# Kernel optimization log

Measured on AMD Instinct MI355X. Metric: run time of the kernel, lower is better.

Reference implementation:

```python
import jax, jax.numpy as jnp
import numpy as np

B = 64        # num_groups
G = 32        # group_size
D = 2000      # output dim (counts per bin/gene)
M = 16        # m_samples
E = 16        # noise_dim
DIN = 256
LAM = 1.0
TRUST = 0.25
SMOOTH = 1e-8
IPF_ITERS = 60
EPS = 1e-12


def _arch(x, noise, W, b):
    # simple linear architecture: concat(x, noise) @ W + b
    return jnp.concatenate([x, noise], axis=-1) @ W + b


def _loss(x, target, W, b, noise_loss):
    # replicate each row m times (unsqueeze(1).expand(...).reshape == repeat)
    x_rep = jnp.repeat(x, M, axis=0)                      # [n*M, DIN]
    pred = _arch(x_rep, noise_loss, W, b)                 # [n*M, D] (no act_fn in loss path)
    pred = pred.reshape(B, G, M, D).sum(axis=1)           # [B, M, D]
    term_conf = jnp.linalg.norm(pred - target[:, None, :], axis=2).mean(axis=1)  # [B]
    sq = jnp.sum(pred * pred, axis=2)                     # [B, M]
    inn = jnp.einsum('bmd,bnd->bmn', pred, pred)          # [B, M, M]
    sqd = jnp.clip(sq[:, :, None] + sq[:, None, :] - 2.0 * inn, 1e-6)
    d = jnp.sqrt(sqd)
    mask = 1.0 - jnp.eye(M, dtype=d.dtype)
    mean_pd = jnp.sum(d * mask, axis=(1, 2)) / (M * (M - 1))
    return jnp.mean(term_conf - (LAM / 2.0) * mean_pd)


def _ipf(x_pred, C):
    # KL/I-projection with row anchoring (keep_rows=True, trust_clip=0.25)
    y = jnp.clip(x_pred, 0.0)
    C = jnp.clip(C.astype(y.dtype), 0.0)
    R = y.sum(axis=2)                                     # [B, G] anchor row totals
    col_zero = (y.sum(axis=1) <= 0) & (C > 0)
    y = y + SMOOTH * col_zero[:, None, :].astype(y.dtype)
    row_zero = (y.sum(axis=2) <= 0) & (R > 0)
    y = y + SMOOTH * row_zero[:, :, None].astype(y.dtype)

    def body(_, y):
        col = jnp.clip(y.sum(axis=1), EPS)
        y = y * jnp.clip(C / col, 1.0 - TRUST, 1.0 + TRUST)[:, None, :]
        row = jnp.clip(y.sum(axis=2), EPS)
        y = y * jnp.clip(R / row, 1.0 - TRUST, 1.0 + TRUST)[:, :, None]
        return y

    y = jax.lax.fori_loop(0, IPF_ITERS, body, y)
    col = jnp.clip(y.sum(axis=1), EPS)
    return y * (C / col)[:, None, :]


def _rank(v, descending):
    # rank along last axis via double argsort (0 = first picked)
    order = jnp.argsort(-v if descending else v, axis=-1)
    return jnp.argsort(order, axis=-1)


def _round_to_targets(x, target_bd):
    # exact integerization across G per (B, D); jit-safe full-G rank replaces dynamic-k topk+scatter
    x = jnp.clip(x, 0.0)
    xf = jnp.floor(x)
    y = xf.astype(jnp.int32)                              # [B, G, D]
    frac = x - xf
    need = target_bd - y.sum(axis=1)                      # [B, D]
    pos = jnp.clip(need, 0)
    q = pos // G
    y = y + q[:, None, :]
    r = pos - q * G
    rank = _rank(jnp.transpose(frac, (0, 2, 1)), descending=True)   # [B, D, G]
    add = (rank < r[:, :, None]).astype(jnp.int32)
    y = y + jnp.transpose(add, (0, 2, 1))
    # negative residuals: remove from smallest frac among y > 0
    need = target_bd - y.sum(axis=1)
    neg = jnp.clip(-need, 0)
    neg = jnp.minimum(neg, y.sum(axis=1))
    q = neg // G
    y_before = y
    y = jnp.clip(y - q[:, None, :], 0)
    removed = (y_before - y).sum(axis=1)
    r = neg - removed
    frac_m = jnp.where(y > 0, frac, jnp.inf)
    rank = _rank(jnp.transpose(frac_m, (0, 2, 1)), descending=False)
    rem = (rank < r[:, :, None]).astype(jnp.int32)
    y = jnp.clip(y - jnp.transpose(rem, (0, 2, 1)), 0)
    return y


def setup_inputs() -> dict:
    key = jax.random.key(0)
    ks = jax.random.split(key, 6)
    x = jax.random.normal(ks[0], (B * G, DIN), dtype=jnp.float32)
    target = jax.random.uniform(ks[1], (B, D), dtype=jnp.float32) * 100.0
    target_sum = jax.random.randint(ks[2], (B, D), 0, 200, dtype=jnp.int32)
    W = jax.random.normal(ks[3], (DIN + E, D), dtype=jnp.float32) * 0.02
    b = jnp.zeros((D,), dtype=jnp.float32)
    noise_loss = jax.random.normal(ks[4], (B * G * M, E), dtype=jnp.float32)
    noise_sample = jax.random.normal(ks[5], (B * G, E), dtype=jnp.float32)
    return {"x": x, "target": target, "target_sum": target_sum, "W": W, "b": b,
            "noise_loss": noise_loss, "noise_sample": noise_sample}


def reference(x, target, target_sum, W, b, noise_loss, noise_sample):
    loss = _loss(x, target, W, b, noise_loss)
    # conditional_sample pipeline (no-grad in original): softplus act (min_value==0)
    x_pred = jax.nn.softplus(_arch(x, noise_sample, W, b)).reshape(B, G, D)
    y_float = _ipf(x_pred, target_sum.astype(jnp.float32))
    y_int = _round_to_targets(y_float, target_sum.astype(jnp.int32))
    return loss, y_int.reshape(B * G, D)
```

## Files before the change

### kernel.cpp

```cpp
#include <hip/hip_runtime.h>
#include <math.h>

#define NB   64
#define NG   32
#define ND   2000
#define NM   16
#define NE   16
#define NDIN 256
#define NK   272

__device__ __forceinline__ float clampf(float v, float lo, float hi) {
    return fminf(fmaxf(v, lo), hi);
}

__device__ __forceinline__ float softplusf(float v) {
    return (v > 20.f) ? v : log1pf(expf(v));
}

__device__ __forceinline__ float readlane_f(float v, int lane) {
    return __int_as_float(__builtin_amdgcn_readlane(__float_as_int(v), lane));
}

__device__ __forceinline__ float wave_sum32(float v[NG], int lane) {
    {   const bool hi = (lane & 32) != 0;
        #pragma unroll
        for (int k = 0; k < 16; ++k) {
            float s = hi ? v[k] : v[k + 16];
            float r = __shfl_xor(s, 32);
            v[k] = (hi ? v[k + 16] : v[k]) + r;
        }
    }
    {   const bool hi = (lane & 16) != 0;
        #pragma unroll
        for (int k = 0; k < 8; ++k) {
            float s = hi ? v[k] : v[k + 8];
            float r = __shfl_xor(s, 16);
            v[k] = (hi ? v[k + 8] : v[k]) + r;
        }
    }
    {   const bool hi = (lane & 8) != 0;
        #pragma unroll
        for (int k = 0; k < 4; ++k) {
            float s = hi ? v[k] : v[k + 4];
            float r = __shfl_xor(s, 8);
            v[k] = (hi ? v[k + 4] : v[k]) + r;
        }
    }
    {   const bool hi = (lane & 4) != 0;
        #pragma unroll
        for (int k = 0; k < 2; ++k) {
            float s = hi ? v[k] : v[k + 2];
            float r = __shfl_xor(s, 4);
            v[k] = (hi ? v[k + 2] : v[k]) + r;
        }
    }
    {   const bool hi = (lane & 2) != 0;
        float s = hi ? v[0] : v[1];
        float r = __shfl_xor(s, 2);
        v[0] = (hi ? v[1] : v[0]) + r;
    }
    v[0] += __shfl_xor(v[0], 1);
    return v[0];
}


__device__ __forceinline__ void ipf_path(
        const float* __restrict__ xp, const int* __restrict__ tsum,
        float* __restrict__ out, float* smem, int b, int t) {
    const int lane = t & 63, w = t >> 6;
    const int d0 = t * 4;
    const bool valid = (d0 < ND);
    const int g_own = (lane >> 1) & 31;

    float* wred = smem;

    float y0r[4][NG];
    #pragma unroll
    for (int g = 0; g < NG; ++g) {
        float4 v = make_float4(0.f, 0.f, 0.f, 0.f);
        if (valid) v = *(const float4*)(xp + (size_t)(b * NG + g) * ND + d0);
        y0r[0][g] = fmaxf(v.x, 0.f);
        y0r[1][g] = fmaxf(v.y, 0.f);
        y0r[2][g] = fmaxf(v.z, 0.f);
        y0r[3][g] = fmaxf(v.w, 0.f);
    }
    float Cc[4] = {0.f, 0.f, 0.f, 0.f};
    if (valid) {
        const int4 ci = *(const int4*)(tsum + (size_t)b * ND + d0);
        Cc[0] = (float)ci.x; Cc[1] = (float)ci.y; Cc[2] = (float)ci.z; Cc[3] = (float)ci.w;
    }
    float Ac[4] = {1.f, 1.f, 1.f, 1.f};
    float Bown = 1.f;
    float Rown;

    {
        float v[NG];
        #pragma unroll
        for (int g = 0; g < NG; ++g)
            v[g] = y0r[0][g] + y0r[1][g] + y0r[2][g] + y0r[3][g];
        const float tot = wave_sum32(v, lane);
        if ((lane & 1) == 0) wred[w * NG + g_own] = tot;
        __syncthreads();
        float s = 0.f;
        #pragma unroll
        for (int w2 = 0; w2 < 8; ++w2) s += wred[w2 * NG + g_own];
        Rown = s;
    }

    for (int q = 1; q <= 60; ++q) {
        float s0 = 0.f, s1 = 0.f, s2 = 0.f, s3 = 0.f;
        #pragma unroll
        for (int g = 0; g < NG; ++g) {
            const float bg = readlane_f(Bown, 2 * g);
            s0 += y0r[0][g] * bg; s1 += y0r[1][g] * bg;
            s2 += y0r[2][g] * bg; s3 += y0r[3][g] * bg;
        }
        Ac[0] *= clampf(Cc[0] / fmaxf(Ac[0] * s0, 1e-12f), 0.75f, 1.25f);
        Ac[1] *= clampf(Cc[1] / fmaxf(Ac[1] * s1, 1e-12f), 0.75f, 1.25f);
        Ac[2] *= clampf(Cc[2] / fmaxf(Ac[2] * s2, 1e-12f), 0.75f, 1.25f);
        Ac[3] *= clampf(Cc[3] / fmaxf(Ac[3] * s3, 1e-12f), 0.75f, 1.25f);
        float v[NG];
        #pragma unroll
        for (int g = 0; g < NG; ++g)
            v[g] = y0r[0][g] * Ac[0] + y0r[1][g] * Ac[1]
                 + y0r[2][g] * Ac[2] + y0r[3][g] * Ac[3];
        const float tot = wave_sum32(v, lane);
        const int buf = (q & 1) * (8 * NG);
        if ((lane & 1) == 0) wred[buf + w * NG + g_own] = tot;
        __syncthreads();
        float s = 0.f;
        #pragma unroll
        for (int w2 = 0; w2 < 8; ++w2) s += wred[buf + w2 * NG + g_own];
        Bown *= clampf(Rown / fmaxf(Bown * s, 1e-12f), 0.75f, 1.25f);
    }

    if (!valid) return;

    unsigned pk[NG];
    #pragma unroll
    for (int g = 0; g < NG; ++g) pk[g] = 0u;

    #pragma unroll
    for (int j = 0; j < 4; ++j) {
        float fr[NG];
        int   yv[NG];
        float s = 0.f;
        #pragma unroll
        for (int g = 0; g < NG; ++g) {
            const float z = y0r[j][g] * Ac[j] * readlane_f(Bown, 2 * g);
            fr[g] = z;
            s += z;
        }
        const float F = Cc[j] / fmaxf(s, 1e-12f);
        int isum = 0;
        #pragma unroll
        for (int g = 0; g < NG; ++g) {
            const float y = fr[g] * F;
            const float fl = floorf(y);
            yv[g] = (int)fl;
            fr[g] = y - fl;
            isum += yv[g];
        }
        const int Ci = (int)Cc[j];
        const int need = Ci - isum;
        const int pos = max(need, 0);
        const int q = pos >> 5;
        const int r = pos & 31;
        #pragma unroll
        for (int g = 0; g < NG; ++g) yv[g] += q;
        #pragma unroll
        for (int g = 0; g < NG; ++g) {
            int rank = 0;
            #pragma unroll
            for (int h = 0; h < NG; ++h) {
                if (h == g) continue;
                rank += (h < g) ? (fr[h] >= fr[g] ? 1 : 0) : (fr[h] > fr[g] ? 1 : 0);
            }
            if (rank < r) yv[g] += 1;
        }
        int neg = max(-need, 0);
        neg = min(neg, isum);
        if (__builtin_expect(neg > 0, 0)) {
            const int q2 = neg >> 5;
            int removed = 0;
            #pragma unroll
            for (int g = 0; g < NG; ++g) {
                const int yb = yv[g];
                const int yn = max(yb - q2, 0);
                removed += yb - yn;
                yv[g] = yn;
            }
            const int r2 = neg - removed;
            if (r2 > 0) {
                const float INF = __builtin_inff();
                #pragma unroll
                for (int g = 0; g < NG; ++g) {
                    const float fg = (yv[g] > 0) ? fr[g] : INF;
                    int rank = 0;
                    #pragma unroll
                    for (int h = 0; h < NG; ++h) {
                        if (h == g) continue;
                        const float fh = (yv[h] > 0) ? fr[h] : INF;
                        rank += (h < g) ? (fh <= fg ? 1 : 0) : (fh < fg ? 1 : 0);
                    }
                    if (rank < r2) yv[g] = max(yv[g] - 1, 0);
                }
            }
        }
        #pragma unroll
        for (int g = 0; g < NG; ++g)
            pk[g] |= ((unsigned)yv[g]) << (8 * j);
    }
    #pragma unroll
    for (int g = 0; g < NG; ++g) {
        float* op = &out[1 + (size_t)(b * NG + g) * ND + d0];
        op[0] = (float)(pk[g] & 0xffu);
        op[1] = (float)((pk[g] >> 8) & 0xffu);
        op[2] = (float)((pk[g] >> 16) & 0xffu);
        op[3] = (float)((pk[g] >> 24) & 0xffu);
    }
}

__device__ __forceinline__ void loss_path(
        const float* __restrict__ x, const float* __restrict__ nl,
        const float* __restrict__ tgt, const float* __restrict__ W,
        const float* __restrict__ bias, float* __restrict__ res2,
        float* smem, int cx, int b, int t) {
    float* xsl = smem;
    float* nsl = smem + 256;
    float* tgl = smem + 512;
    float* pt  = smem + 764;

    if (t < 256) {
        const float* xb = x + (size_t)b * NG * NDIN;
        float s = 0.f;
        for (int g = 0; g < NG; ++g) s += xb[g * NDIN + t];
        xsl[t] = s;
        const float* nb = nl + (size_t)b * NG * (NM * NE);
        float s2 = 0.f;
        for (int g = 0; g < NG; ++g) s2 += nb[g * (NM * NE) + t];
        nsl[t] = s2;
    }

    int tm = 0, tn = 0;
    if (t >= 16 && t < 152) {
        int p = t - 16;
        for (int m = 0; m < NM; ++m) {
            int c = NM - m;
            if (p < c) { tm = m; tn = m + p; break; }
            p -= c;
        }
    }
    __syncthreads();

    const int d = cx * 250 + t;
    if (t < 250) {
        tgl[t] = tgt[b * ND + d];
        float xw = 0.f;
        #pragma unroll 8
        for (int k = 0; k < NDIN; ++k) xw += xsl[k] * W[(size_t)k * ND + d];
        float we[NE];
        #pragma unroll
        for (int e = 0; e < NE; ++e) we[e] = W[(size_t)(NDIN + e) * ND + d];
        const float base0 = xw + (float)NG * bias[d];
        #pragma unroll
        for (int m = 0; m < NM; ++m) {
            float pm = base0;
            #pragma unroll
            for (int e = 0; e < NE; ++e) pm += nsl[m * NE + e] * we[e];
            pt[m * 252 + t] = pm;
        }
    }
    if (t < 32) {
        pt[(t >> 1) * 252 + 250 + (t & 1)] = 0.f;
        if (t < 2) tgl[250 + t] = 0.f;
    }
    __syncthreads();

    float acc = 0.f;
    if (t < 16) {
        const float4* pa  = (const float4*)&pt[t * 252];
        const float4* tga = (const float4*)&tgl[0];
        for (int i = 0; i < 63; ++i) {
            float4 pv = pa[i], tv = tga[i];
            float e0 = pv.x - tv.x, e1 = pv.y - tv.y, e2 = pv.z - tv.z, e3 = pv.w - tv.w;
            acc += e0 * e0 + e1 * e1 + e2 * e2 + e3 * e3;
        }
    } else if (t < 152) {
        const float4* pa = (const float4*)&pt[tm * 252];
        const float4* pb = (const float4*)&pt[tn * 252];
        for (int i = 0; i < 63; ++i) {
            float4 u = pa[i], v = pb[i];
            acc += u.x * v.x + u.y * v.y + u.z * v.z + u.w * v.w;
        }
    }
    if (t < 152) res2[((size_t)b * 8 + cx) * 152 + t] = acc;
}

extern "C" __global__ __launch_bounds__(512, 1)
void mega(const float* __restrict__ x, const float* __restrict__ nl,
          const float* __restrict__ tgt, const float* __restrict__ W,
          const float* __restrict__ bias, const float* __restrict__ xp,
          const int* __restrict__ tsum, float* __restrict__ out,
          float* __restrict__ res2) {
    __shared__ float smem[4800];
    const int bid = blockIdx.x;
    const int t = threadIdx.x;
    if (bid < NB) {
        ipf_path(xp, tsum, out, smem, bid, t);
    } else {
        const int q = bid - NB;
        loss_path(x, nl, tgt, W, bias, res2, smem, q & 7, q >> 3, t);
    }
}

extern "C" __global__ __launch_bounds__(64)
void k2b_combine(const float* __restrict__ res2, float* __restrict__ out) {
    const int b = blockIdx.x, t = threadIdx.x;
    __shared__ float res[152];
    for (int tau = t; tau < 152; tau += 64) {
        float s = 0.f;
        #pragma unroll
        for (int c = 0; c < 8; ++c) s += res2[((size_t)b * 8 + c) * 152 + tau];
        res[tau] = s;
    }
    __syncthreads();
    if (t == 0) {
        float conf = 0.f;
        for (int m = 0; m < NM; ++m) conf += sqrtf(res[m]);
        conf *= (1.f / NM);
        float pd = 0.f;
        for (int m = 0; m < NM; ++m) {
            const int offm = 16 + m * NM - m * (m - 1) / 2;
            const float sqm = res[offm];
            for (int n = m + 1; n < NM; ++n) {
                const int offn = 16 + n * NM - n * (n - 1) / 2;
                const float sqn = res[offn];
                const float inn = res[offm + (n - m)];
                pd += sqrtf(fmaxf(sqm + sqn - 2.f * inn, 1e-6f));
            }
        }
        pd = 2.f * pd / (float)(NM * (NM - 1));
        atomicAdd(out, (conf - 0.5f * pd) * (1.f / NB));
    }
}

extern "C" __global__ __launch_bounds__(256)
void k3_xpred(const float* __restrict__ x, const float* __restrict__ nsamp,
              const float* __restrict__ W, const float* __restrict__ bias,
              float* __restrict__ xp) {
    const int dx = blockIdx.x;
    const int rb = blockIdx.y;
    const int t  = threadIdx.x;
    __shared__ float xr[8][NK];
    #pragma unroll
    for (int r = 0; r < 8; ++r) {
        const int row = rb * 8 + r;
        xr[r][t] = x[(size_t)row * NDIN + t];
        if (t < NE) xr[r][NDIN + t] = nsamp[row * NE + t];
    }
    __syncthreads();
    if (t >= 250) return;
    const int d = dx * 1000 + 4 * t;
    float acc[8][4];
    #pragma unroll
    for (int r = 0; r < 8; ++r) {
        acc[r][0] = 0.f; acc[r][1] = 0.f; acc[r][2] = 0.f; acc[r][3] = 0.f;
    }
    for (int k = 0; k < NK; k += 4) {
        float4 w[4];
        #pragma unroll
        for (int kk = 0; kk < 4; ++kk) w[kk] = *(const float4*)&W[(size_t)(k + kk) * ND + d];
        #pragma unroll
        for (int r = 0; r < 8; ++r) {
            const float4 xv = *(const float4*)&xr[r][k];
            acc[r][0] += xv.x * w[0].x + xv.y * w[1].x + xv.z * w[2].x + xv.w * w[3].x;
            acc[r][1] += xv.x * w[0].y + xv.y * w[1].y + xv.z * w[2].y + xv.w * w[3].y;
            acc[r][2] += xv.x * w[0].z + xv.y * w[1].z + xv.z * w[2].z + xv.w * w[3].z;
            acc[r][3] += xv.x * w[0].w + xv.y * w[1].w + xv.z * w[2].w + xv.w * w[3].w;
        }
    }
    const float4 bv = *(const float4*)&bias[d];
    #pragma unroll
    for (int r = 0; r < 8; ++r) {
        float4 o;
        o.x = softplusf(acc[r][0] + bv.x);
        o.y = softplusf(acc[r][1] + bv.y);
        o.z = softplusf(acc[r][2] + bv.z);
        o.w = softplusf(acc[r][3] + bv.w);
        *(float4*)&xp[(size_t)(rb * 8 + r) * ND + d] = o;
    }
}

extern "C" void kernel_launch(void* const* d_in, const int* in_sizes, int n_in,
                              void* d_out, int out_size, void* d_ws, size_t ws_size,
                              hipStream_t stream) {
    const float* x     = (const float*)d_in[0];
    const float* tgt   = (const float*)d_in[1];
    const int*   tsum  = (const int*)d_in[2];
    const float* W     = (const float*)d_in[3];
    const float* bias  = (const float*)d_in[4];
    const float* nl    = (const float*)d_in[5];
    const float* nsamp = (const float*)d_in[6];
    float* out = (float*)d_out;
    float* xp  = (float*)d_ws;

    (void)in_sizes; (void)n_in; (void)out_size; (void)ws_size;

    const size_t XPB = (size_t)2048 * 2000 * 4;
    float* res2 = (float*)((char*)d_ws + XPB);

    hipMemsetAsync(d_out, 0, sizeof(float), stream);

    hipLaunchKernelGGL(k3_xpred, dim3(2, 256), dim3(256), 0, stream,
                       x, nsamp, W, bias, xp);
    hipLaunchKernelGGL(mega, dim3(NB + 512), dim3(512), 0, stream,
                       x, nl, tgt, W, bias, xp, tsum, out, res2);
    hipLaunchKernelGGL(k2b_combine, dim3(NB), dim3(64), 0, stream, res2, out);
}
```

Baseline: 318.5 us.

## Double block size to 1024 threads, two columns per thread in IPF

The fused kernel now runs 1024-thread blocks. In the IPF path each thread owns 2 columns instead of 4, which halves the per-thread register arrays and the serial FMA chains across the 60 iterations. The cross-wave reduction now spans 16 waves. In the loss path each 1024-thread block packs two former 512-thread column chunks that share the group sums in shared memory. The cost is a larger __syncthreads barrier and more shared-memory reads per IPF iteration, plus a waves-per-EU hint that caps registers.

```diff
diff --git a/kernel.cpp b/kernel.cpp
--- a/kernel.cpp
+++ b/kernel.cpp
@@ -8,6 +8,7 @@
 #define NE   16
 #define NDIN 256
 #define NK   272
+#define NWAVES 16
 
 __device__ __forceinline__ float clampf(float v, float lo, float hi) {
     return fminf(fmaxf(v, lo), hi);
@@ -68,28 +69,26 @@
         const float* __restrict__ xp, const int* __restrict__ tsum,
         float* __restrict__ out, float* smem, int b, int t) {
     const int lane = t & 63, w = t >> 6;
-    const int d0 = t * 4;
+    const int d0 = t * 2;
     const bool valid = (d0 < ND);
     const int g_own = (lane >> 1) & 31;
 
     float* wred = smem;
 
-    float y0r[4][NG];
+    float y0r[2][NG];
     #pragma unroll
     for (int g = 0; g < NG; ++g) {
-        float4 v = make_float4(0.f, 0.f, 0.f, 0.f);
-        if (valid) v = *(const float4*)(xp + (size_t)(b * NG + g) * ND + d0);
+        float2 v = make_float2(0.f, 0.f);
+        if (valid) v = *(const float2*)(xp + (size_t)(b * NG + g) * ND + d0);
         y0r[0][g] = fmaxf(v.x, 0.f);
         y0r[1][g] = fmaxf(v.y, 0.f);
-        y0r[2][g] = fmaxf(v.z, 0.f);
-        y0r[3][g] = fmaxf(v.w, 0.f);
-    }
-    float Cc[4] = {0.f, 0.f, 0.f, 0.f};
+    }
+    float Cc[2] = {0.f, 0.f};
     if (valid) {
-        const int4 ci = *(const int4*)(tsum + (size_t)b * ND + d0);
-        Cc[0] = (float)ci.x; Cc[1] = (float)ci.y; Cc[2] = (float)ci.z; Cc[3] = (float)ci.w;
-    }
-    float Ac[4] = {1.f, 1.f, 1.f, 1.f};
+        const int2 ci = *(const int2*)(tsum + (size_t)b * ND + d0);
+        Cc[0] = (float)ci.x; Cc[1] = (float)ci.y;
+    }
+    float Ac[2] = {1.f, 1.f};
     float Bown = 1.f;
     float Rown;
 
@@ -97,40 +96,36 @@
         float v[NG];
         #pragma unroll
         for (int g = 0; g < NG; ++g)
-            v[g] = y0r[0][g] + y0r[1][g] + y0r[2][g] + y0r[3][g];
+            v[g] = y0r[0][g] + y0r[1][g];
         const float tot = wave_sum32(v, lane);
         if ((lane & 1) == 0) wred[w * NG + g_own] = tot;
         __syncthreads();
         float s = 0.f;
         #pragma unroll
-        for (int w2 = 0; w2 < 8; ++w2) s += wred[w2 * NG + g_own];
+        for (int w2 = 0; w2 < NWAVES; ++w2) s += wred[w2 * NG + g_own];
         Rown = s;
     }
 
     for (int q = 1; q <= 60; ++q) {
-        float s0 = 0.f, s1 = 0.f, s2 = 0.f, s3 = 0.f;
+        float s0 = 0.f, s1 = 0.f;
         #pragma unroll
         for (int g = 0; g < NG; ++g) {
             const float bg = readlane_f(Bown, 2 * g);
             s0 += y0r[0][g] * bg; s1 += y0r[1][g] * bg;
-            s2 += y0r[2][g] * bg; s3 += y0r[3][g] * bg;
         }
         Ac[0] *= clampf(Cc[0] / fmaxf(Ac[0] * s0, 1e-12f), 0.75f, 1.25f);
         Ac[1] *= clampf(Cc[1] / fmaxf(Ac[1] * s1, 1e-12f), 0.75f, 1.25f);
-        Ac[2] *= clampf(Cc[2] / fmaxf(Ac[2] * s2, 1e-12f), 0.75f, 1.25f);
-        Ac[3] *= clampf(Cc[3] / fmaxf(Ac[3] * s3, 1e-12f), 0.75f, 1.25f);
         float v[NG];
         #pragma unroll
         for (int g = 0; g < NG; ++g)
-            v[g] = y0r[0][g] * Ac[0] + y0r[1][g] * Ac[1]
-                 + y0r[2][g] * Ac[2] + y0r[3][g] * Ac[3];
+            v[g] = y0r[0][g] * Ac[0] + y0r[1][g] * Ac[1];
         const float tot = wave_sum32(v, lane);
-        const int buf = (q & 1) * (8 * NG);
+        const int buf = (q & 1) * (NWAVES * NG);
         if ((lane & 1) == 0) wred[buf + w * NG + g_own] = tot;
         __syncthreads();
         float s = 0.f;
         #pragma unroll
-        for (int w2 = 0; w2 < 8; ++w2) s += wred[buf + w2 * NG + g_own];
+        for (int w2 = 0; w2 < NWAVES; ++w2) s += wred[buf + w2 * NG + g_own];
         Bown *= clampf(Rown / fmaxf(Bown * s, 1e-12f), 0.75f, 1.25f);
     }
 
@@ -141,7 +136,7 @@
     for (int g = 0; g < NG; ++g) pk[g] = 0u;
 
     #pragma unroll
-    for (int j = 0; j < 4; ++j) {
+    for (int j = 0; j < 2; ++j) {
         float fr[NG];
         int   yv[NG];
         float s = 0.f;
@@ -164,10 +159,10 @@
         const int Ci = (int)Cc[j];
         const int need = Ci - isum;
         const int pos = max(need, 0);
-        const int q = pos >> 5;
+        const int qq = pos >> 5;
         const int r = pos & 31;
         #pragma unroll
-        for (int g = 0; g < NG; ++g) yv[g] += q;
+        for (int g = 0; g < NG; ++g) yv[g] += qq;
         #pragma unroll
         for (int g = 0; g < NG; ++g) {
             int rank = 0;
@@ -216,8 +211,6 @@
         float* op = &out[1 + (size_t)(b * NG + g) * ND + d0];
         op[0] = (float)(pk[g] & 0xffu);
         op[1] = (float)((pk[g] >> 8) & 0xffu);
-        op[2] = (float)((pk[g] >> 16) & 0xffu);
-        op[3] = (float)((pk[g] >> 24) & 0xffu);
     }
 }
 
@@ -225,26 +218,27 @@
         const float* __restrict__ x, const float* __restrict__ nl,
         const float* __restrict__ tgt, const float* __restrict__ W,
         const float* __restrict__ bias, float* __restrict__ res2,
-        float* smem, int cx, int b, int t) {
+        float* smem, int cx, int b, int tt) {
+    const int half = cx & 1;
     float* xsl = smem;
     float* nsl = smem + 256;
-    float* tgl = smem + 512;
-    float* pt  = smem + 764;
-
-    if (t < 256) {
+    float* tgl = smem + 512 + half * 4284;
+    float* pt  = tgl + 252;
+
+    if (half == 0 && tt < 256) {
         const float* xb = x + (size_t)b * NG * NDIN;
         float s = 0.f;
-        for (int g = 0; g < NG; ++g) s += xb[g * NDIN + t];
-        xsl[t] = s;
+        for (int g = 0; g < NG; ++g) s += xb[g * NDIN + tt];
+        xsl[tt] = s;
         const float* nb = nl + (size_t)b * NG * (NM * NE);
         float s2 = 0.f;
-        for (int g = 0; g < NG; ++g) s2 += nb[g * (NM * NE) + t];
-        nsl[t] = s2;
+        for (int g = 0; g < NG; ++g) s2 += nb[g * (NM * NE) + tt];
+        nsl[tt] = s2;
     }
 
     int tm = 0, tn = 0;
-    if (t >= 16 && t < 152) {
-        int p = t - 16;
+    if (tt >= 16 && tt < 152) {
+        int p = tt - 16;
         for (int m = 0; m < NM; ++m) {
             int c = NM - m;
             if (p < c) { tm = m; tn = m + p; break; }
@@ -253,9 +247,9 @@
     }
     __syncthreads();
 
-    const int d = cx * 250 + t;
-    if (t < 250) {
-        tgl[t] = tgt[b * ND + d];
+    const int d = cx * 250 + tt;
+    if (tt < 250) {
+        tgl[tt] = tgt[b * ND + d];
         float xw = 0.f;
         #pragma unroll 8
         for (int k = 0; k < NDIN; ++k) xw += xsl[k] * W[(size_t)k * ND + d];
@@ -268,25 +262,25 @@
             float pm = base0;
             #pragma unroll
             for (int e = 0; e < NE; ++e) pm += nsl[m * NE + e] * we[e];
-            pt[m * 252 + t] = pm;
-        }
-    }
-    if (t < 32) {
-        pt[(t >> 1) * 252 + 250 + (t & 1)] = 0.f;
-        if (t < 2) tgl[250 + t] = 0.f;
+            pt[m * 252 + tt] = pm;
+        }
+    }
+    if (tt < 32) {
+        pt[(tt >> 1) * 252 + 250 + (tt & 1)] = 0.f;
+        if (tt < 2) tgl[250 + tt] = 0.f;
     }
     __syncthreads();
 
     float acc = 0.f;
-    if (t < 16) {
-        const float4* pa  = (const float4*)&pt[t * 252];
+    if (tt < 16) {
+        const float4* pa  = (const float4*)&pt[tt * 252];
         const float4* tga = (const float4*)&tgl[0];
         for (int i = 0; i < 63; ++i) {
             float4 pv = pa[i], tv = tga[i];
             float e0 = pv.x - tv.x, e1 = pv.y - tv.y, e2 = pv.z - tv.z, e3 = pv.w - tv.w;
             acc += e0 * e0 + e1 * e1 + e2 * e2 + e3 * e3;
         }
-    } else if (t < 152) {
+    } else if (tt < 152) {
         const float4* pa = (const float4*)&pt[tm * 252];
         const float4* pb = (const float4*)&pt[tn * 252];
         for (int i = 0; i < 63; ++i) {
@@ -294,23 +288,26 @@
             acc += u.x * v.x + u.y * v.y + u.z * v.z + u.w * v.w;
         }
     }
-    if (t < 152) res2[((size_t)b * 8 + cx) * 152 + t] = acc;
-}
-
-extern "C" __global__ __launch_bounds__(512, 1)
+    if (tt < 152) res2[((size_t)b * 8 + cx) * 152 + tt] = acc;
+}
+
+extern "C" __global__ __launch_bounds__(1024)
+__attribute__((amdgpu_waves_per_eu(4, 4)))
 void mega(const float* __restrict__ x, const float* __restrict__ nl,
           const float* __restrict__ tgt, const float* __restrict__ W,
           const float* __restrict__ bias, const float* __restrict__ xp,
           const int* __restrict__ tsum, float* __restrict__ out,
           float* __restrict__ res2) {
-    __shared__ float smem[4800];
+    __shared__ float smem[9080];
     const int bid = blockIdx.x;
     const int t = threadIdx.x;
     if (bid < NB) {
         ipf_path(xp, tsum, out, smem, bid, t);
     } else {
         const int q = bid - NB;
-        loss_path(x, nl, tgt, W, bias, res2, smem, q & 7, q >> 3, t);
+        const int b = q >> 2;
+        const int cx = ((q & 3) << 1) | (t >> 9);
+        loss_path(x, nl, tgt, W, bias, res2, smem, cx, b, t & 511);
     }
 }
 
@@ -414,7 +411,7 @@
 
     hipLaunchKernelGGL(k3_xpred, dim3(2, 256), dim3(256), 0, stream,
                        x, nsamp, W, bias, xp);
-    hipLaunchKernelGGL(mega, dim3(NB + 512), dim3(512), 0, stream,
+    hipLaunchKernelGGL(mega, dim3(NB + 256), dim3(1024), 0, stream,
                        x, nl, tgt, W, bias, xp, tsum, out, res2);
     hipLaunchKernelGGL(k2b_combine, dim3(NB), dim3(64), 0, stream, res2, out);
 }
```

Result: slower. 336.0 us (+5.5%).

## Stage IPF data in LDS/transposed layout, split rounding into separate epilogue kernel

Applied to the files above, without the earlier changes.

The xpred kernel now writes its output in a transposed, group-major layout. The first 1024 columns go to a plain transposed buffer and the rest to a swizzled side buffer. The IPF loop no longer holds all 128 values per thread in registers: half the threads keep their column chunk in large dynamic LDS, the rest stream it from global memory on every iteration. The rounding step moves to a new k_epi kernel that reads the column and row scale factors through the output buffer, and the loss blocks are folded into 192 blocks that each loop over several tiles. The aim is to cut register pressure and raise occupancy, at the cost of repeated global reads, a large LDS footprint and one extra launch.

```diff
diff --git a/kernel.cpp b/kernel.cpp
--- a/kernel.cpp
+++ b/kernel.cpp
@@ -9,6 +9,11 @@
 #define NDIN 256
 #define NK   272
 
+#define XPT_COLS 1024
+#define SP_STRIDE 7808
+#define SMEM_MEGA (2048 + XPT_COLS * 128)
+#define SMEM_EPI  (128 + 256 * 256)
+
 __device__ __forceinline__ float clampf(float v, float lo, float hi) {
     return fminf(fmaxf(v, lo), hi);
 }
@@ -19,6 +24,12 @@
 
 __device__ __forceinline__ float readlane_f(float v, int lane) {
     return __int_as_float(__builtin_amdgcn_readlane(__float_as_int(v), lane));
+}
+
+__device__ __forceinline__ size_t sp_idx(int tau, int cj, int k) {
+    return (tau < 192)
+        ? ((size_t)((tau >> 6) * 2048 + cj * 512 + k * 64 + (tau & 63)))
+        : ((size_t)(6144 + cj * 416 + k * 52 + (tau - 192)));
 }
 
 __device__ __forceinline__ float wave_sum32(float v[NG], int lane) {
@@ -63,43 +74,66 @@
     return v[0];
 }
 
-
 __device__ __forceinline__ void ipf_path(
-        const float* __restrict__ xp, const int* __restrict__ tsum,
-        float* __restrict__ out, float* smem, int b, int t) {
+        const float* __restrict__ xpT, const float* __restrict__ spB,
+        const int* __restrict__ tsum, float* __restrict__ out,
+        char* smem, int b, int t) {
     const int lane = t & 63, w = t >> 6;
-    const int d0 = t * 4;
-    const bool valid = (d0 < ND);
+    const int c0 = 4 * t;
+    const bool valid = (t < 500);
+    const bool lcls  = (t < 256);
     const int g_own = (lane >> 1) & 31;
-
-    float* wred = smem;
-
-    float y0r[4][NG];
-    #pragma unroll
-    for (int g = 0; g < NG; ++g) {
-        float4 v = make_float4(0.f, 0.f, 0.f, 0.f);
-        if (valid) v = *(const float4*)(xp + (size_t)(b * NG + g) * ND + d0);
-        y0r[0][g] = fmaxf(v.x, 0.f);
-        y0r[1][g] = fmaxf(v.y, 0.f);
-        y0r[2][g] = fmaxf(v.z, 0.f);
-        y0r[3][g] = fmaxf(v.w, 0.f);
-    }
+    const int rot = t & 7;
+    const int tau = t - 256;
+
+    float* wred = (float*)smem;
+    char* cbase = smem + 2048 + (size_t)c0 * 128;
+    const float4* gx = (const float4*)(xpT + ((size_t)b * XPT_COLS + c0) * NG);
+    const float4* gs = (const float4*)(spB + (size_t)b * SP_STRIDE * 4);
+
     float Cc[4] = {0.f, 0.f, 0.f, 0.f};
     if (valid) {
-        const int4 ci = *(const int4*)(tsum + (size_t)b * ND + d0);
-        Cc[0] = (float)ci.x; Cc[1] = (float)ci.y; Cc[2] = (float)ci.z; Cc[3] = (float)ci.w;
+        const int4 ci = *(const int4*)(tsum + (size_t)b * ND + c0);
+        Cc[0] = (float)ci.x; Cc[1] = (float)ci.y;
+        Cc[2] = (float)ci.z; Cc[3] = (float)ci.w;
     }
     float Ac[4] = {1.f, 1.f, 1.f, 1.f};
-    float Bown = 1.f;
-    float Rown;
+    float Bown = 1.f, Rown;
 
     {
         float v[NG];
-        #pragma unroll
-        for (int g = 0; g < NG; ++g)
-            v[g] = y0r[0][g] + y0r[1][g] + y0r[2][g] + y0r[3][g];
+        if (lcls) {
+            #pragma unroll
+            for (int k = 0; k < 8; ++k) {
+                const float4 a = gx[k], e = gx[8 + k], f = gx[16 + k], h = gx[24 + k];
+                const int ro = 16 * ((k + rot) & 7);
+                *(float4*)(cbase + ro)       = a;
+                *(float4*)(cbase + 128 + ro) = e;
+                *(float4*)(cbase + 256 + ro) = f;
+                *(float4*)(cbase + 384 + ro) = h;
+                v[4*k+0] = ((a.x + e.x) + f.x) + h.x;
+                v[4*k+1] = ((a.y + e.y) + f.y) + h.y;
+                v[4*k+2] = ((a.z + e.z) + f.z) + h.z;
+                v[4*k+3] = ((a.w + e.w) + f.w) + h.w;
+            }
+        } else if (valid) {
+            #pragma unroll
+            for (int k = 0; k < 8; ++k) {
+                const float4 a = gs[sp_idx(tau, 0, k)];
+                const float4 e = gs[sp_idx(tau, 1, k)];
+                const float4 f = gs[sp_idx(tau, 2, k)];
+                const float4 h = gs[sp_idx(tau, 3, k)];
+                v[4*k+0] = ((a.x + e.x) + f.x) + h.x;
+                v[4*k+1] = ((a.y + e.y) + f.y) + h.y;
+                v[4*k+2] = ((a.z + e.z) + f.z) + h.z;
+                v[4*k+3] = ((a.w + e.w) + f.w) + h.w;
+            }
+        } else {
+            #pragma unroll
+            for (int g = 0; g < NG; ++g) v[g] = 0.f;
+        }
         const float tot = wave_sum32(v, lane);
-        if ((lane & 1) == 0) wred[w * NG + g_own] = tot;
+        if (!(lane & 1)) wred[w * NG + g_own] = tot;
         __syncthreads();
         float s = 0.f;
         #pragma unroll
@@ -109,24 +143,74 @@
 
     for (int q = 1; q <= 60; ++q) {
         float s0 = 0.f, s1 = 0.f, s2 = 0.f, s3 = 0.f;
-        #pragma unroll
-        for (int g = 0; g < NG; ++g) {
-            const float bg = readlane_f(Bown, 2 * g);
-            s0 += y0r[0][g] * bg; s1 += y0r[1][g] * bg;
-            s2 += y0r[2][g] * bg; s3 += y0r[3][g] * bg;
+        if (lcls) {
+            #pragma unroll
+            for (int k = 0; k < 8; ++k) {
+                const int ro = 16 * ((k + rot) & 7);
+                const float4 a = *(const float4*)(cbase + ro);
+                const float4 e = *(const float4*)(cbase + 128 + ro);
+                const float4 f = *(const float4*)(cbase + 256 + ro);
+                const float4 h = *(const float4*)(cbase + 384 + ro);
+                float bg;
+                bg = readlane_f(Bown, 8*k+0); s0 += a.x*bg; s1 += e.x*bg; s2 += f.x*bg; s3 += h.x*bg;
+                bg = readlane_f(Bown, 8*k+2); s0 += a.y*bg; s1 += e.y*bg; s2 += f.y*bg; s3 += h.y*bg;
+                bg = readlane_f(Bown, 8*k+4); s0 += a.z*bg; s1 += e.z*bg; s2 += f.z*bg; s3 += h.z*bg;
+                bg = readlane_f(Bown, 8*k+6); s0 += a.w*bg; s1 += e.w*bg; s2 += f.w*bg; s3 += h.w*bg;
+            }
+        } else if (valid) {
+            #pragma unroll
+            for (int k = 0; k < 8; ++k) {
+                const float4 a = gs[sp_idx(tau, 0, k)];
+                const float4 e = gs[sp_idx(tau, 1, k)];
+                const float4 f = gs[sp_idx(tau, 2, k)];
+                const float4 h = gs[sp_idx(tau, 3, k)];
+                float bg;
+                bg = readlane_f(Bown, 8*k+0); s0 += a.x*bg; s1 += e.x*bg; s2 += f.x*bg; s3 += h.x*bg;
+                bg = readlane_f(Bown, 8*k+2); s0 += a.y*bg; s1 += e.y*bg; s2 += f.y*bg; s3 += h.y*bg;
+                bg = readlane_f(Bown, 8*k+4); s0 += a.z*bg; s1 += e.z*bg; s2 += f.z*bg; s3 += h.z*bg;
+                bg = readlane_f(Bown, 8*k+6); s0 += a.w*bg; s1 += e.w*bg; s2 += f.w*bg; s3 += h.w*bg;
+            }
         }
         Ac[0] *= clampf(Cc[0] / fmaxf(Ac[0] * s0, 1e-12f), 0.75f, 1.25f);
         Ac[1] *= clampf(Cc[1] / fmaxf(Ac[1] * s1, 1e-12f), 0.75f, 1.25f);
         Ac[2] *= clampf(Cc[2] / fmaxf(Ac[2] * s2, 1e-12f), 0.75f, 1.25f);
         Ac[3] *= clampf(Cc[3] / fmaxf(Ac[3] * s3, 1e-12f), 0.75f, 1.25f);
+
+        asm volatile("" ::: "memory");
+
         float v[NG];
-        #pragma unroll
-        for (int g = 0; g < NG; ++g)
-            v[g] = y0r[0][g] * Ac[0] + y0r[1][g] * Ac[1]
-                 + y0r[2][g] * Ac[2] + y0r[3][g] * Ac[3];
+        if (lcls) {
+            #pragma unroll
+            for (int k = 0; k < 8; ++k) {
+                const int ro = 16 * ((k + rot) & 7);
+                const float4 a = *(const float4*)(cbase + ro);
+                const float4 e = *(const float4*)(cbase + 128 + ro);
+                const float4 f = *(const float4*)(cbase + 256 + ro);
+                const float4 h = *(const float4*)(cbase + 384 + ro);
+                v[4*k+0] = a.x*Ac[0] + e.x*Ac[1] + f.x*Ac[2] + h.x*Ac[3];
+                v[4*k+1] = a.y*Ac[0] + e.y*Ac[1] + f.y*Ac[2] + h.y*Ac[3];
+                v[4*k+2] = a.z*Ac[0] + e.z*Ac[1] + f.z*Ac[2] + h.z*Ac[3];
+                v[4*k+3] = a.w*Ac[0] + e.w*Ac[1] + f.w*Ac[2] + h.w*Ac[3];
+            }
+        } else if (valid) {
+            #pragma unroll
+            for (int k = 0; k < 8; ++k) {
+                const float4 a = gs[sp_idx(tau, 0, k)];
+                const float4 e = gs[sp_idx(tau, 1, k)];
+                const float4 f = gs[sp_idx(tau, 2, k)];
+                const float4 h = gs[sp_idx(tau, 3, k)];
+                v[4*k+0] = a.x*Ac[0] + e.x*Ac[1] + f.x*Ac[2] + h.x*Ac[3];
+                v[4*k+1] = a.y*Ac[0] + e.y*Ac[1] + f.y*Ac[2] + h.y*Ac[3];
+                v[4*k+2] = a.z*Ac[0] + e.z*Ac[1] + f.z*Ac[2] + h.z*Ac[3];
+                v[4*k+3] = a.w*Ac[0] + e.w*Ac[1] + f.w*Ac[2] + h.w*Ac[3];
+            }
+        } else {
+            #pragma unroll
+            for (int g = 0; g < NG; ++g) v[g] = 0.f;
+        }
         const float tot = wave_sum32(v, lane);
         const int buf = (q & 1) * (8 * NG);
-        if ((lane & 1) == 0) wred[buf + w * NG + g_own] = tot;
+        if (!(lane & 1)) wred[buf + w * NG + g_own] = tot;
         __syncthreads();
         float s = 0.f;
         #pragma unroll
@@ -134,90 +218,14 @@
         Bown *= clampf(Rown / fmaxf(Bown * s, 1e-12f), 0.75f, 1.25f);
     }
 
-    if (!valid) return;
-
-    unsigned pk[NG];
-    #pragma unroll
-    for (int g = 0; g < NG; ++g) pk[g] = 0u;
-
-    #pragma unroll
-    for (int j = 0; j < 4; ++j) {
-        float fr[NG];
-        int   yv[NG];
-        float s = 0.f;
-        #pragma unroll
-        for (int g = 0; g < NG; ++g) {
-            const float z = y0r[j][g] * Ac[j] * readlane_f(Bown, 2 * g);
-            fr[g] = z;
-            s += z;
-        }
-        const float F = Cc[j] / fmaxf(s, 1e-12f);
-        int isum = 0;
-        #pragma unroll
-        for (int g = 0; g < NG; ++g) {
-            const float y = fr[g] * F;
-            const float fl = floorf(y);
-            yv[g] = (int)fl;
-            fr[g] = y - fl;
-            isum += yv[g];
-        }
-        const int Ci = (int)Cc[j];
-        const int need = Ci - isum;
-        const int pos = max(need, 0);
-        const int q = pos >> 5;
-        const int r = pos & 31;
-        #pragma unroll
-        for (int g = 0; g < NG; ++g) yv[g] += q;
-        #pragma unroll
-        for (int g = 0; g < NG; ++g) {
-            int rank = 0;
-            #pragma unroll
-            for (int h = 0; h < NG; ++h) {
-                if (h == g) continue;
-                rank += (h < g) ? (fr[h] >= fr[g] ? 1 : 0) : (fr[h] > fr[g] ? 1 : 0);
-            }
-            if (rank < r) yv[g] += 1;
-        }
-        int neg = max(-need, 0);
-        neg = min(neg, isum);
-        if (__builtin_expect(neg > 0, 0)) {
-            const int q2 = neg >> 5;
-            int removed = 0;
-            #pragma unroll
-            for (int g = 0; g < NG; ++g) {
-                const int yb = yv[g];
-                const int yn = max(yb - q2, 0);
-                removed += yb - yn;
-                yv[g] = yn;
-            }
-            const int r2 = neg - removed;
-            if (r2 > 0) {
-                const float INF = __builtin_inff();
-                #pragma unroll
-                for (int g = 0; g < NG; ++g) {
-                    const float fg = (yv[g] > 0) ? fr[g] : INF;
-                    int rank = 0;
-                    #pragma unroll
-                    for (int h = 0; h < NG; ++h) {
-                        if (h == g) continue;
-                        const float fh = (yv[h] > 0) ? fr[h] : INF;
-                        rank += (h < g) ? (fh <= fg ? 1 : 0) : (fh < fg ? 1 : 0);
-                    }
-                    if (rank < r2) yv[g] = max(yv[g] - 1, 0);
-                }
-            }
-        }
-        #pragma unroll
-        for (int g = 0; g < NG; ++g)
-            pk[g] |= ((unsigned)yv[g]) << (8 * j);
-    }
-    #pragma unroll
-    for (int g = 0; g < NG; ++g) {
-        float* op = &out[1 + (size_t)(b * NG + g) * ND + d0];
-        op[0] = (float)(pk[g] & 0xffu);
-        op[1] = (float)((pk[g] >> 8) & 0xffu);
-        op[2] = (float)((pk[g] >> 16) & 0xffu);
-        op[3] = (float)((pk[g] >> 24) & 0xffu);
+    if (valid) {
+        float* ap = out + 1 + (size_t)(b * NG) * ND + c0;
+        ap[0] = Ac[0]; ap[1] = Ac[1]; ap[2] = Ac[2]; ap[3] = Ac[3];
+    }
+    if (w == 0 && !(lane & 1)) {
+        #pragma unroll
+        for (int qq = 0; qq < 4; ++qq)
+            out[1 + (size_t)(b * NG + 1) * ND + qq * 500 + g_own] = Bown;
     }
 }
 
@@ -297,20 +305,144 @@
     if (t < 152) res2[((size_t)b * 8 + cx) * 152 + t] = acc;
 }
 
-extern "C" __global__ __launch_bounds__(512, 1)
+extern "C" __global__ __launch_bounds__(512)
 void mega(const float* __restrict__ x, const float* __restrict__ nl,
           const float* __restrict__ tgt, const float* __restrict__ W,
-          const float* __restrict__ bias, const float* __restrict__ xp,
-          const int* __restrict__ tsum, float* __restrict__ out,
-          float* __restrict__ res2) {
-    __shared__ float smem[4800];
+          const float* __restrict__ bias, const float* __restrict__ xpT,
+          const float* __restrict__ spB, const int* __restrict__ tsum,
+          float* __restrict__ out, float* __restrict__ res2) {
+    extern __shared__ char smem[];
     const int bid = blockIdx.x;
     const int t = threadIdx.x;
     if (bid < NB) {
-        ipf_path(xp, tsum, out, smem, bid, t);
+        ipf_path(xpT, spB, tsum, out, smem, bid, t);
     } else {
-        const int q = bid - NB;
-        loss_path(x, nl, tgt, W, bias, res2, smem, q & 7, q >> 3, t);
+        const int l = bid - NB;
+        #pragma unroll
+        for (int rep = 0; rep < 3; ++rep) {
+            const int p = l + rep * 192;
+            if (p < 512) {
+                __syncthreads();
+                loss_path(x, nl, tgt, W, bias, res2, (float*)smem,
+                          p & 7, p >> 3, t);
+            }
+        }
+    }
+}
+
+extern "C" __global__ __launch_bounds__(256)
+void k_epi(const float* __restrict__ xpT, const float* __restrict__ spB,
+           const int* __restrict__ tsum, float* __restrict__ out) {
+    extern __shared__ char smem[];
+    const int bid = blockIdx.x;
+    const int b = bid >> 2, qq = bid & 3;
+    const int tt = threadIdx.x;
+    float* bf  = (float*)smem;
+    float* epf = (float*)(smem + 128 + (size_t)tt * 256);
+    int*   epy = (int*)(smem + 128 + (size_t)tt * 256 + 128);
+
+    if (tt < 32)
+        bf[tt] = out[1 + (size_t)(b * NG + 1) * ND + qq * 500 + tt];
+    __syncthreads();
+    if (tt >= 250) return;
+
+    const int d0 = qq * 500 + 2 * tt;
+    const float A0 = out[1 + (size_t)(b * NG) * ND + d0];
+    const float A1 = out[1 + (size_t)(b * NG) * ND + d0 + 1];
+    const int2 ci = *(const int2*)(tsum + (size_t)b * ND + d0);
+    const float Cc[2] = {(float)ci.x, (float)ci.y};
+    const float Aj[2] = {A0, A1};
+
+    #pragma unroll
+    for (int j = 0; j < 2; ++j) {
+        const int c = d0 + j;
+        float4 ch[8];
+        if (c < XPT_COLS) {
+            const float4* cp = (const float4*)(xpT + ((size_t)b * XPT_COLS + c) * NG);
+            #pragma unroll
+            for (int k = 0; k < 8; ++k) ch[k] = cp[k];
+        } else {
+            const float4* gsp = (const float4*)(spB + (size_t)b * SP_STRIDE * 4);
+            const int tau2 = (c - XPT_COLS) >> 2, cj = (c - XPT_COLS) & 3;
+            #pragma unroll
+            for (int k = 0; k < 8; ++k) ch[k] = gsp[sp_idx(tau2, cj, k)];
+        }
+        float s = 0.f;
+        #pragma unroll
+        for (int k = 0; k < 8; ++k) {
+            float z;
+            z = ch[k].x * Aj[j] * bf[4*k+0]; s += z; epf[(4*k+0+tt)&31] = z;
+            z = ch[k].y * Aj[j] * bf[4*k+1]; s += z; epf[(4*k+1+tt)&31] = z;
+            z = ch[k].z * Aj[j] * bf[4*k+2]; s += z; epf[(4*k+2+tt)&31] = z;
+            z = ch[k].w * Aj[j] * bf[4*k+3]; s += z; epf[(4*k+3+tt)&31] = z;
+        }
+        const float F = Cc[j] / fmaxf(s, 1e-12f);
+        int isum = 0;
+        #pragma unroll
+        for (int g = 0; g < NG; ++g) {
+            const float y = epf[(g+tt)&31] * F;
+            const float fl = floorf(y);
+            const int yi = (int)fl;
+            epf[(g+tt)&31] = y - fl;
+            epy[(g+tt)&31] = yi;
+            isum += yi;
+        }
+        const int Ci = (int)Cc[j];
+        const int need = Ci - isum;
+        const int pos = max(need, 0);
+        const int qv = pos >> 5;
+        const int rr = pos & 31;
+        if (qv > 0) {
+            #pragma unroll
+            for (int g = 0; g < NG; ++g) epy[(g+tt)&31] += qv;
+        }
+        #pragma unroll
+        for (int g = 0; g < NG; ++g) {
+            const float fg = epf[(g+tt)&31];
+            int rank = 0;
+            #pragma unroll
+            for (int h = 0; h < NG; ++h) {
+                if (h == g) continue;
+                const float fh = epf[(h+tt)&31];
+                rank += (h < g) ? (fh >= fg ? 1 : 0) : (fh > fg ? 1 : 0);
+            }
+            if (rank < rr) epy[(g+tt)&31] += 1;
+        }
+        int neg = max(-need, 0);
+        neg = min(neg, isum);
+        if (__builtin_expect(neg > 0, 0)) {
+            const int q2 = neg >> 5;
+            int removed = 0;
+            #pragma unroll
+            for (int g = 0; g < NG; ++g) {
+                const int yb = epy[(g+tt)&31];
+                const int yn = max(yb - q2, 0);
+                removed += yb - yn;
+                epy[(g+tt)&31] = yn;
+            }
+            const int r2 = neg - removed;
+            if (r2 > 0) {
+                const float INF = __builtin_inff();
+                #pragma unroll
+                for (int g = 0; g < NG; ++g) {
+                    const float fg = (epy[(g+tt)&31] > 0) ? epf[(g+tt)&31] : INF;
+                    int rank = 0;
+                    #pragma unroll
+                    for (int h = 0; h < NG; ++h) {
+                        if (h == g) continue;
+                        const float fh = (epy[(h+tt)&31] > 0) ? epf[(h+tt)&31] : INF;
+                        rank += (h < g) ? (fh <= fg ? 1 : 0) : (fh < fg ? 1 : 0);
+                    }
+                    if (rank < r2) {
+                        const int yb = epy[(g+tt)&31];
+                        epy[(g+tt)&31] = max(yb - 1, 0);
+                    }
+                }
+            }
+        }
+        #pragma unroll
+        for (int g = 0; g < NG; ++g)
+            out[1 + (size_t)(b * NG + g) * ND + d0 + j] = (float)epy[(g+tt)&31];
     }
 }
 
@@ -348,7 +480,7 @@
 extern "C" __global__ __launch_bounds__(256)
 void k3_xpred(const float* __restrict__ x, const float* __restrict__ nsamp,
               const float* __restrict__ W, const float* __restrict__ bias,
-              float* __restrict__ xp) {
+              float* __restrict__ xpT, float* __restrict__ spB) {
     const int dx = blockIdx.x;
     const int rb = blockIdx.y;
     const int t  = threadIdx.x;
@@ -381,14 +513,32 @@
         }
     }
     const float4 bv = *(const float4*)&bias[d];
+    const float bvv[4] = {bv.x, bv.y, bv.z, bv.w};
+    const int b2 = rb >> 2;
+    const int g0 = (rb & 3) * 8;
     #pragma unroll
-    for (int r = 0; r < 8; ++r) {
-        float4 o;
-        o.x = softplusf(acc[r][0] + bv.x);
-        o.y = softplusf(acc[r][1] + bv.y);
-        o.z = softplusf(acc[r][2] + bv.z);
-        o.w = softplusf(acc[r][3] + bv.w);
-        *(float4*)&xp[(size_t)(rb * 8 + r) * ND + d] = o;
+    for (int dd = 0; dd < 4; ++dd) {
+        const int dc = d + dd;
+        float4 lo, hi;
+        lo.x = softplusf(acc[0][dd] + bvv[dd]);
+        lo.y = softplusf(acc[1][dd] + bvv[dd]);
+        lo.z = softplusf(acc[2][dd] + bvv[dd]);
+        lo.w = softplusf(acc[3][dd] + bvv[dd]);
+        hi.x = softplusf(acc[4][dd] + bvv[dd]);
+        hi.y = softplusf(acc[5][dd] + bvv[dd]);
+        hi.z = softplusf(acc[6][dd] + bvv[dd]);
+        hi.w = softplusf(acc[7][dd] + bvv[dd]);
+        if (dc < XPT_COLS) {
+            float* op = xpT + ((size_t)b2 * XPT_COLS + dc) * NG + g0;
+            *(float4*)op       = lo;
+            *(float4*)(op + 4) = hi;
+        } else {
+            float4* sp = (float4*)spB + (size_t)b2 * SP_STRIDE;
+            const int tau2 = (dc - XPT_COLS) >> 2, cj = (dc - XPT_COLS) & 3;
+            const int kk = g0 >> 2;
+            sp[sp_idx(tau2, cj, kk)]     = lo;
+            sp[sp_idx(tau2, cj, kk + 1)] = hi;
+        }
     }
 }
 
@@ -403,18 +553,31 @@
     const float* nl    = (const float*)d_in[5];
     const float* nsamp = (const float*)d_in[6];
     float* out = (float*)d_out;
-    float* xp  = (float*)d_ws;
 
     (void)in_sizes; (void)n_in; (void)out_size; (void)ws_size;
 
-    const size_t XPB = (size_t)2048 * 2000 * 4;
-    float* res2 = (float*)((char*)d_ws + XPB);
+    float* xpT  = (float*)d_ws;
+    float* spB  = (float*)((char*)d_ws + 8388608);
+    float* res2 = (float*)((char*)d_ws + 16384000);
+
+    static int s_attr_done = 0;
+    if (!s_attr_done) {
+        hipFuncSetAttribute(reinterpret_cast<const void*>(mega),
+                            hipFuncAttributeMaxDynamicSharedMemorySize,
+                            SMEM_MEGA);
+        hipFuncSetAttribute(reinterpret_cast<const void*>(k_epi),
+                            hipFuncAttributeMaxDynamicSharedMemorySize,
+                            SMEM_EPI);
+        s_attr_done = 1;
+    }
 
     hipMemsetAsync(d_out, 0, sizeof(float), stream);
 
     hipLaunchKernelGGL(k3_xpred, dim3(2, 256), dim3(256), 0, stream,
-                       x, nsamp, W, bias, xp);
-    hipLaunchKernelGGL(mega, dim3(NB + 512), dim3(512), 0, stream,
-                       x, nl, tgt, W, bias, xp, tsum, out, res2);
+                       x, nsamp, W, bias, xpT, spB);
+    hipLaunchKernelGGL(mega, dim3(256), dim3(512), SMEM_MEGA, stream,
+                       x, nl, tgt, W, bias, xpT, spB, tsum, out, res2);
+    hipLaunchKernelGGL(k_epi, dim3(256), dim3(256), SMEM_EPI, stream,
+                       xpT, spB, tsum, out);
     hipLaunchKernelGGL(k2b_combine, dim3(NB), dim3(64), 0, stream, res2, out);
 }
```

Result: slower. 414.7 us (+30.2%).
